# Optimization experiments

Hardware: AMD Instinct MI355X
Metric: run time of the kernel (lower is better)

## Reference

```python
import jax, jax.numpy as jnp
import numpy as np


def setup_inputs() -> dict:
    key = jax.random.key(0)
    kq, kk, kv = jax.random.split(key, 3)
    B, Lq, Lk, D = 4, 4096, 4096, 64
    return {
        "Q": jax.random.normal(kq, (B, Lq, D), dtype=jnp.float32),
        "K": jax.random.normal(kk, (B, Lk, D), dtype=jnp.float32),
        "V": jax.random.normal(kv, (B, Lk, D), dtype=jnp.float32),
    }


def reference(Q, K, V):
    # scores: [B, Lq, Lk]  (no 1/sqrt(d) scaling in the original module)
    scores = jnp.einsum("bqd,bkd->bqk", Q, K)
    attn = jax.nn.softmax(scores, axis=-1)
    # output: [B, Lq, D]
    return jnp.einsum("bqk,bkd->bqd", attn, V)
```

## Files before the change

kernel.cpp:

```cpp
#include <hip/hip_runtime.h>
#include <cmath>


#define B_    4
#define LQ    4096
#define LK    4096
#define DH    64
#define BQ    128
#define NQT2  (B_ * LQ / BQ)
#define NKVT  (LK / 128)
#define NROWS (B_ * LQ)
#define LOG2E 1.44269504088896f
#define C0    63.4785817991f

typedef _Float16 f16x8 __attribute__((ext_vector_type(8)));
typedef _Float16 f16x4 __attribute__((ext_vector_type(4)));
typedef float    f32x4 __attribute__((ext_vector_type(4)));
typedef short    s16x8 __attribute__((ext_vector_type(8)));
typedef int      i32x4 __attribute__((ext_vector_type(4)));

__device__ inline float exp2_(float x) {
#if __has_builtin(__builtin_amdgcn_exp2f)
  return __builtin_amdgcn_exp2f(x);
#else
  return exp2f(x);
#endif
}

__device__ inline unsigned pkbf16(float lo, float hi) {
  return __builtin_amdgcn_perm(__float_as_uint(hi), __float_as_uint(lo),
                               0x07060302u);
}

__device__ inline unsigned short bf16rne(float f) {
  unsigned u = __float_as_uint(f);
  return (unsigned short)((u + 0x7FFF + ((u >> 16) & 1)) >> 16);
}

__device__ inline void async16(const void* g, void* l) {
  __builtin_amdgcn_global_load_lds(
      (const __attribute__((address_space(1))) unsigned int*)g,
      (__attribute__((address_space(3))) unsigned int*)l, 16, 0, 0);
}

__global__ __launch_bounds__(256) void convert_kv4(
    const float* __restrict__ K, const float* __restrict__ V,
    _Float16* __restrict__ Kh, unsigned short* __restrict__ Vb) {
  __shared__ unsigned short Vs[64 * 68];
  const int tid = threadIdx.x;
  const int bb = blockIdx.x;
  const bool isV = bb >= 256;
  const int cc = isV ? bb - 256 : bb;
  const int b = cc >> 6, tile = (cc >> 1) & 31, half = cc & 1;
  const int kv0 = tile * 128 + half * 64;

  if (!isV) {
    for (int i = 0; i < 2; ++i) {
      int q = i * 256 + tid;
      int r = q >> 3, g = q & 7;
      const float* src = K + ((size_t)(b * LK + kv0 + r)) * DH + g * 8;
      float4 a = *(const float4*)src;
      float4 d = *(const float4*)(src + 4);
      f16x8 hv = {(_Float16)(a.x), (_Float16)(a.y), (_Float16)(a.z), (_Float16)(a.w),
                  (_Float16)(d.x), (_Float16)(d.y), (_Float16)(d.z), (_Float16)(d.w)};
      int gp = g ^ (r & 7);
      size_t dst = ((size_t)(b * 32 + tile) * 128 + half * 64 + r) * 64 + gp * 8;
      *(f16x8*)(&Kh[dst]) = hv;
    }
  } else {
    for (int i = 0; i < 4; ++i) {
      int idx = i * 256 + tid;
      int vr = idx >> 4, c4 = idx & 15;
      float4 v = *(const float4*)(&V[((size_t)(b * LK + kv0 + vr)) * DH + c4 * 4]);
      Vs[vr * 68 + c4 * 4 + 0] = bf16rne(v.x);
      Vs[vr * 68 + c4 * 4 + 1] = bf16rne(v.y);
      Vs[vr * 68 + c4 * 4 + 2] = bf16rne(v.z);
      Vs[vr * 68 + c4 * 4 + 3] = bf16rne(v.w);
    }
    __syncthreads();
    for (int i = 0; i < 2; ++i) {
      int q = i * 256 + tid;
      int d = q >> 3, gl = q & 7;
      int g = half * 8 + gl;
      unsigned short ov[8];
#pragma unroll
      for (int j = 0; j < 8; ++j) {
        int p = g * 8 + j;
        int c = p >> 5, w5 = p & 31;
        int qd = w5 >> 3, jj = w5 & 7, hh = jj >> 2, r = jj & 3;
        int sL = 32 * c + 16 * hh + 4 * qd + r - 64 * half;
        ov[j] = Vs[sL * 68 + d];
      }
      int gp = g ^ (d & 7);
      size_t dst = ((size_t)(b * 32 + tile) * 64 + d) * 128 + gp * 8;
      s16x8 o8;
#pragma unroll
      for (int j = 0; j < 8; ++j) o8[j] = (short)ov[j];
      *(s16x8*)(&Vb[dst]) = o8;
    }
  }
}

__global__ __launch_bounds__(256, 4) void ca_flash4(
    const float* __restrict__ Q, const _Float16* __restrict__ Kh,
    const unsigned short* __restrict__ Vb, float* __restrict__ Out,
    _Float16* __restrict__ Opart, float* __restrict__ Lw, int nsplit) {
  __shared__ _Float16 KsH[128 * 64];
  __shared__ unsigned short VtH[64 * 128];

  const int tid  = threadIdx.x;
  const int wave = tid >> 6;
  const int lane = tid & 63;
  const int quad = lane >> 4;
  const int l16  = lane & 15;
  const int e    = quad ^ (l16 & 7);

  const int qt    = blockIdx.x;
  const int b     = qt >> 5;
  const int qbase = (qt & 31) * BQ;
  const int sp    = blockIdx.y;
  const int t0 = (NKVT * sp) / nsplit;
  const int t1 = (NKVT * (sp + 1)) / nsplit;

  f16x8 qf[2][2];
#pragma unroll
  for (int sub = 0; sub < 2; ++sub) {
    int qrow = qbase + wave * 32 + sub * 16 + l16;
    const float* qp = Q + ((size_t)b * LQ + qrow) * DH + quad * 8;
#pragma unroll
    for (int kk = 0; kk < 2; ++kk) {
      float4 a = *(const float4*)(qp + kk * 32);
      float4 c = *(const float4*)(qp + kk * 32 + 4);
      f16x8 f = {(_Float16)(a.x * LOG2E), (_Float16)(a.y * LOG2E),
                 (_Float16)(a.z * LOG2E), (_Float16)(a.w * LOG2E),
                 (_Float16)(c.x * LOG2E), (_Float16)(c.y * LOG2E),
                 (_Float16)(c.z * LOG2E), (_Float16)(c.w * LOG2E)};
      qf[sub][kk] = f;
    }
  }

  f32x4 o[2][5];
#pragma unroll
  for (int sub = 0; sub < 2; ++sub)
#pragma unroll
    for (int td = 0; td < 5; ++td) o[sub][td] = (f32x4){0.f, 0.f, 0.f, 0.f};

  s16x8 ones;
#pragma unroll
  for (int j = 0; j < 8; ++j) ones[j] = (short)0x3F80;

  const char* kg = (const char*)Kh + ((size_t)(b * 32 + t0)) * 16384;
  const char* vg = (const char*)Vb + ((size_t)(b * 32 + t0)) * 16384;
  char* ksB = (char*)KsH;
  char* vtB = (char*)VtH;
  const char* kR = ksB + l16 * 128;
  const char* vR = vtB + l16 * 256;

  for (int tile = t0; tile < t1; ++tile) {
    __syncthreads();
    const char* sg = (wave < 2) ? (kg + wave * 8192) : (vg + (wave - 2) * 8192);
    char*       sd = (wave < 2) ? (ksB + wave * 8192) : (vtB + (wave - 2) * 8192);
#pragma unroll
    for (int i = 0; i < 8; ++i) async16(sg + i * 1024 + lane * 16, sd + i * 1024);
    __syncthreads();
    kg += 16384; vg += 16384;

#pragma unroll
    for (int c = 0; c < 4; ++c) {
      f32x4 sv[2][2];
#pragma unroll
      for (int sub = 0; sub < 2; ++sub)
#pragma unroll
        for (int tt = 0; tt < 2; ++tt)
          sv[sub][tt] = (f32x4){-C0, -C0, -C0, -C0};
#pragma unroll
      for (int kk = 0; kk < 2; ++kk) {
        int ko = (e ^ (4 * kk)) * 16;
#pragma unroll
        for (int tt = 0; tt < 2; ++tt) {
          f16x8 bk = *(const f16x8*)(kR + (2 * c + tt) * 2048 + ko);
          sv[0][tt] = __builtin_amdgcn_mfma_f32_16x16x32_f16(bk, qf[0][kk], sv[0][tt], 0, 0, 0);
          sv[1][tt] = __builtin_amdgcn_mfma_f32_16x16x32_f16(bk, qf[1][kk], sv[1][tt], 0, 0, 0);
        }
      }

      s16x8 ap[2];
#pragma unroll
      for (int sub = 0; sub < 2; ++sub) {
        unsigned u0 = pkbf16(exp2_(sv[sub][0][0]), exp2_(sv[sub][0][1]));
        unsigned u1 = pkbf16(exp2_(sv[sub][0][2]), exp2_(sv[sub][0][3]));
        unsigned u2 = pkbf16(exp2_(sv[sub][1][0]), exp2_(sv[sub][1][1]));
        unsigned u3 = pkbf16(exp2_(sv[sub][1][2]), exp2_(sv[sub][1][3]));
        i32x4 iv = {(int)u0, (int)u1, (int)u2, (int)u3};
        ap[sub] = __builtin_bit_cast(s16x8, iv);
      }

      int vo = (e ^ (4 * c)) * 16;
#pragma unroll
      for (int td = 0; td < 4; ++td) {
        s16x8 bv = *(const s16x8*)(vR + td * 4096 + vo);
        o[0][td] = __builtin_amdgcn_mfma_f32_16x16x32_bf16(ap[0], bv, o[0][td], 0, 0, 0);
        o[1][td] = __builtin_amdgcn_mfma_f32_16x16x32_bf16(ap[1], bv, o[1][td], 0, 0, 0);
      }
      o[0][4] = __builtin_amdgcn_mfma_f32_16x16x32_bf16(ap[0], ones, o[0][4], 0, 0, 0);
      o[1][4] = __builtin_amdgcn_mfma_f32_16x16x32_bf16(ap[1], ones, o[1][4], 0, 0, 0);
    }
  }

  if (nsplit == 1) {
#pragma unroll
    for (int sub = 0; sub < 2; ++sub)
#pragma unroll
      for (int r = 0; r < 4; ++r) {
        float inv = 1.0f / (o[sub][4][r] + 1e-35f);
        size_t row = (size_t)b * LQ + qbase + wave * 32 + sub * 16 + quad * 4 + r;
#pragma unroll
        for (int td = 0; td < 4; ++td)
          Out[row * DH + td * 16 + l16] = o[sub][td][r] * inv;
      }
  } else {
#pragma unroll
    for (int sub = 0; sub < 2; ++sub)
#pragma unroll
      for (int r = 0; r < 4; ++r) {
        float l = o[sub][4][r];
        float inv = 1.0f / (l + 1e-35f);
        size_t g = (size_t)qt * BQ + wave * 32 + sub * 16 + quad * 4 + r;
        size_t prow = (size_t)sp * NROWS + g;
#pragma unroll
        for (int td = 0; td < 4; ++td)
          Opart[prow * DH + td * 16 + l16] = (_Float16)(o[sub][td][r] * inv);
        if (l16 == 0) Lw[prow] = l;
      }
  }
}

__global__ __launch_bounds__(256) void ca_combine4(
    const _Float16* __restrict__ Opart, const float* __restrict__ Lw,
    float* __restrict__ Out, int nsplit) {
  const int idx = blockIdx.x * 256 + threadIdx.x;
  const int g = idx >> 4;
  const int c0 = (idx & 15) * 4;
  float den = 1e-30f;
  float a0 = 0.f, a1 = 0.f, a2 = 0.f, a3 = 0.f;
  for (int s = 0; s < nsplit; ++s) {
    size_t prow = (size_t)s * NROWS + g;
    float w = Lw[prow];
    f16x4 v = *(const f16x4*)(&Opart[prow * DH + c0]);
    a0 += w * (float)v[0]; a1 += w * (float)v[1];
    a2 += w * (float)v[2]; a3 += w * (float)v[3];
    den += w;
  }
  float inv = 1.0f / den;
  float4 ov = {a0 * inv, a1 * inv, a2 * inv, a3 * inv};
  *(float4*)(&Out[(size_t)g * DH + c0]) = ov;
}

#define LDSS 72
__global__ __launch_bounds__(256) void ca_flash_naive(
    const float* __restrict__ Q, const float* __restrict__ K,
    const float* __restrict__ V, float* __restrict__ Out) {
  __shared__ _Float16 Qs[64 * LDSS];
  __shared__ _Float16 Ks[64 * LDSS];
  __shared__ _Float16 Vt[64 * LDSS];
  __shared__ _Float16 Ps[64 * LDSS];
  const int tid = threadIdx.x, wave = tid >> 6, lane = tid & 63;
  const int quad = lane >> 4, l16 = lane & 15;
  const int b = blockIdx.x >> 6, qbase = (blockIdx.x & 63) * 64;
  for (int i = 0; i < 4; ++i) {
    int idx = (i * 256 + tid) * 4;
    int r = idx >> 6, c = idx & 63;
    float4 q4 = *(const float4*)(&Q[((size_t)b * LQ + qbase + r) * DH + c]);
    f16x4 hh = {(_Float16)q4.x, (_Float16)q4.y, (_Float16)q4.z, (_Float16)q4.w};
    *(f16x4*)(&Qs[r * LDSS + c]) = hh;
  }
  __syncthreads();
  f16x8 qf[2];
  qf[0] = *(const f16x8*)(&Qs[(wave * 16 + l16) * LDSS + quad * 8]);
  qf[1] = *(const f16x8*)(&Qs[(wave * 16 + l16) * LDSS + quad * 8 + 32]);
  float m_i[4], l_i[4];
  f32x4 o[4];
  for (int r = 0; r < 4; ++r) {
    m_i[r] = -INFINITY; l_i[r] = 0.f; o[r] = (f32x4){0.f, 0.f, 0.f, 0.f};
  }
  for (int kv0 = 0; kv0 < LK; kv0 += 64) {
    __syncthreads();
    for (int i = 0; i < 4; ++i) {
      int idx = (i * 256 + tid) * 4;
      int r = idx >> 6, c = idx & 63;
      float4 k4 = *(const float4*)(&K[((size_t)b * LK + kv0 + r) * DH + c]);
      f16x4 hh = {(_Float16)k4.x, (_Float16)k4.y, (_Float16)k4.z, (_Float16)k4.w};
      *(f16x4*)(&Ks[r * LDSS + c]) = hh;
      float4 v4 = *(const float4*)(&V[((size_t)b * LK + kv0 + r) * DH + c]);
      Vt[(c + 0) * LDSS + r] = (_Float16)v4.x;
      Vt[(c + 1) * LDSS + r] = (_Float16)v4.y;
      Vt[(c + 2) * LDSS + r] = (_Float16)v4.z;
      Vt[(c + 3) * LDSS + r] = (_Float16)v4.w;
    }
    __syncthreads();
    f32x4 sv[4];
    for (int t = 0; t < 4; ++t) sv[t] = (f32x4){0.f, 0.f, 0.f, 0.f};
    for (int kk = 0; kk < 2; ++kk)
      for (int t = 0; t < 4; ++t) {
        f16x8 bk = *(const f16x8*)(&Ks[(t * 16 + l16) * LDSS + quad * 8 + kk * 32]);
        sv[t] = __builtin_amdgcn_mfma_f32_16x16x32_f16(qf[kk], bk, sv[t], 0, 0, 0);
      }
    for (int r = 0; r < 4; ++r) {
      float mx = fmaxf(fmaxf(sv[0][r], sv[1][r]), fmaxf(sv[2][r], sv[3][r]));
      for (int off = 1; off < 16; off <<= 1) mx = fmaxf(mx, __shfl_xor(mx, off, 64));
      float mnew = fmaxf(m_i[r], mx);
      float alpha = __expf(m_i[r] - mnew);
      float rs = 0.f;
      for (int t = 0; t < 4; ++t) { float p = __expf(sv[t][r] - mnew); sv[t][r] = p; rs += p; }
      for (int off = 1; off < 16; off <<= 1) rs += __shfl_xor(rs, off, 64);
      l_i[r] = l_i[r] * alpha + rs;
      m_i[r] = mnew;
      for (int td = 0; td < 4; ++td) o[td][r] *= alpha;
    }
    for (int t = 0; t < 4; ++t)
      for (int r = 0; r < 4; ++r)
        Ps[(wave * 16 + quad * 4 + r) * LDSS + t * 16 + l16] = (_Float16)sv[t][r];
    for (int kk = 0; kk < 2; ++kk) {
      f16x8 ap = *(const f16x8*)(&Ps[(wave * 16 + l16) * LDSS + quad * 8 + kk * 32]);
      for (int td = 0; td < 4; ++td) {
        f16x8 bv = *(const f16x8*)(&Vt[(td * 16 + l16) * LDSS + quad * 8 + kk * 32]);
        o[td] = __builtin_amdgcn_mfma_f32_16x16x32_f16(ap, bv, o[td], 0, 0, 0);
      }
    }
  }
  float inv_l[4];
  for (int r = 0; r < 4; ++r) inv_l[r] = 1.0f / l_i[r];
  for (int td = 0; td < 4; ++td)
    for (int r = 0; r < 4; ++r) {
      size_t row = (size_t)b * LQ + qbase + wave * 16 + quad * 4 + r;
      Out[row * DH + td * 16 + l16] = o[td][r] * inv_l[r];
    }
}

extern "C" void kernel_launch(void* const* d_in, const int* in_sizes, int n_in,
                              void* d_out, int out_size, void* d_ws, size_t ws_size,
                              hipStream_t stream) {
  const float* Q = (const float*)d_in[0];
  const float* K = (const float*)d_in[1];
  const float* V = (const float*)d_in[2];
  float* Out = (float*)d_out;

  const size_t sKh = (size_t)B_ * LK * DH * sizeof(_Float16);
  const size_t sVb = (size_t)B_ * LK * DH * sizeof(unsigned short);
  const size_t base = sKh + sVb;
  auto opSize = [](int sp) { return (size_t)sp * NROWS * DH * sizeof(_Float16); };
  auto lwSize = [](int sp) { return (size_t)sp * NROWS * sizeof(float); };

  int split = 0;
  if (base + opSize(8) + lwSize(8) <= ws_size) split = 8;
  else if (base + opSize(6) + lwSize(6) <= ws_size) split = 6;
  else if (base + opSize(4) + lwSize(4) <= ws_size) split = 4;
  else if (base + opSize(2) + lwSize(2) <= ws_size) split = 2;
  else if (base <= ws_size) split = 1;

  char* ws = (char*)d_ws;
  if (split >= 1) {
    _Float16* Kh = (_Float16*)ws;
    unsigned short* Vb = (unsigned short*)(ws + sKh);
    convert_kv4<<<dim3(512), dim3(256), 0, stream>>>(K, V, Kh, Vb);
    if (split == 1) {
      ca_flash4<<<dim3(NQT2, 1), dim3(256), 0, stream>>>(
          Q, Kh, Vb, Out, nullptr, nullptr, 1);
    } else {
      _Float16* Op = (_Float16*)(ws + base);
      float* Lwp = (float*)(ws + base + opSize(split));
      ca_flash4<<<dim3(NQT2, split), dim3(256), 0, stream>>>(
          Q, Kh, Vb, Out, Op, Lwp, split);
      ca_combine4<<<dim3(NROWS * DH / 4 / 256), dim3(256), 0, stream>>>(
          Op, Lwp, Out, split);
    }
  } else {
    ca_flash_naive<<<dim3(256), dim3(256), 0, stream>>>(Q, K, V, Out);
  }
}
```

Before: 97.00 us.

## Fuse split-KV combine into flash kernel via last-block atomic counter

Removes the separate combine kernel launch. Each split block writes its partial output, then bumps a per-query-tile atomic counter, and the last block to arrive performs the weighted reduction into the final output. This saves one kernel launch and its dependency gap, at the cost of a memset launch, threadfences, and a serialized combine tail in the last-arriving block.

```diff
diff --git a/kernel.cpp b/kernel.cpp
--- a/kernel.cpp
+++ b/kernel.cpp
@@ -101,12 +101,14 @@
   }
 }
 
-__global__ __launch_bounds__(256, 4) void ca_flash4(
+__global__ __launch_bounds__(256, 4) void ca_flash6(
     const float* __restrict__ Q, const _Float16* __restrict__ Kh,
     const unsigned short* __restrict__ Vb, float* __restrict__ Out,
-    _Float16* __restrict__ Opart, float* __restrict__ Lw, int nsplit) {
+    _Float16* __restrict__ Opart, float* __restrict__ Lw,
+    int* __restrict__ done, int nsplit) {
   __shared__ _Float16 KsH[128 * 64];
   __shared__ unsigned short VtH[64 * 128];
+  __shared__ int sh_st;
 
   const int tid  = threadIdx.x;
   const int wave = tid >> 6;
@@ -218,42 +220,50 @@
         for (int td = 0; td < 4; ++td)
           Out[row * DH + td * 16 + l16] = o[sub][td][r] * inv;
       }
-  } else {
-#pragma unroll
-    for (int sub = 0; sub < 2; ++sub)
-#pragma unroll
-      for (int r = 0; r < 4; ++r) {
-        float l = o[sub][4][r];
-        float inv = 1.0f / (l + 1e-35f);
-        size_t g = (size_t)qt * BQ + wave * 32 + sub * 16 + quad * 4 + r;
-        size_t prow = (size_t)sp * NROWS + g;
-#pragma unroll
-        for (int td = 0; td < 4; ++td)
-          Opart[prow * DH + td * 16 + l16] = (_Float16)(o[sub][td][r] * inv);
-        if (l16 == 0) Lw[prow] = l;
-      }
-  }
-}
-
-__global__ __launch_bounds__(256) void ca_combine4(
-    const _Float16* __restrict__ Opart, const float* __restrict__ Lw,
-    float* __restrict__ Out, int nsplit) {
-  const int idx = blockIdx.x * 256 + threadIdx.x;
-  const int g = idx >> 4;
-  const int c0 = (idx & 15) * 4;
-  float den = 1e-30f;
-  float a0 = 0.f, a1 = 0.f, a2 = 0.f, a3 = 0.f;
-  for (int s = 0; s < nsplit; ++s) {
-    size_t prow = (size_t)s * NROWS + g;
-    float w = Lw[prow];
-    f16x4 v = *(const f16x4*)(&Opart[prow * DH + c0]);
-    a0 += w * (float)v[0]; a1 += w * (float)v[1];
-    a2 += w * (float)v[2]; a3 += w * (float)v[3];
-    den += w;
-  }
-  float inv = 1.0f / den;
-  float4 ov = {a0 * inv, a1 * inv, a2 * inv, a3 * inv};
-  *(float4*)(&Out[(size_t)g * DH + c0]) = ov;
+    return;
+  }
+
+#pragma unroll
+  for (int sub = 0; sub < 2; ++sub)
+#pragma unroll
+    for (int r = 0; r < 4; ++r) {
+      float l = o[sub][4][r];
+      float inv = 1.0f / (l + 1e-35f);
+      size_t g = (size_t)qt * BQ + wave * 32 + sub * 16 + quad * 4 + r;
+      size_t prow = (size_t)sp * NROWS + g;
+#pragma unroll
+      for (int td = 0; td < 4; ++td)
+        Opart[prow * DH + td * 16 + l16] = (_Float16)(o[sub][td][r] * inv);
+      if (l16 == 0) Lw[prow] = l;
+    }
+
+  __threadfence();
+  __syncthreads();
+  if (tid == 0)
+    sh_st = __hip_atomic_fetch_add(done + qt, 1, __ATOMIC_ACQ_REL,
+                                   __HIP_MEMORY_SCOPE_AGENT);
+  __syncthreads();
+  if (sh_st == nsplit - 1) {
+    __threadfence();
+    for (int i = 0; i < 8; ++i) {
+      int idx = i * 256 + tid;
+      int rr = idx >> 4;
+      int c0 = (idx & 15) * 4;
+      size_t g = (size_t)qt * BQ + rr;
+      float den = 1e-30f, a0 = 0.f, a1 = 0.f, a2 = 0.f, a3 = 0.f;
+      for (int s2 = 0; s2 < nsplit; ++s2) {
+        size_t prow = (size_t)s2 * NROWS + g;
+        float w = Lw[prow];
+        f16x4 v = *(const f16x4*)(&Opart[prow * DH + c0]);
+        a0 += w * (float)v[0]; a1 += w * (float)v[1];
+        a2 += w * (float)v[2]; a3 += w * (float)v[3];
+        den += w;
+      }
+      float inv = 1.0f / den;
+      float4 ov = {a0 * inv, a1 * inv, a2 * inv, a3 * inv};
+      *(float4*)(&Out[g * DH + c0]) = ov;
+    }
+  }
 }
 
 #define LDSS 72
@@ -350,12 +360,13 @@
   const size_t base = sKh + sVb;
   auto opSize = [](int sp) { return (size_t)sp * NROWS * DH * sizeof(_Float16); };
   auto lwSize = [](int sp) { return (size_t)sp * NROWS * sizeof(float); };
+  const size_t sDone = NQT2 * sizeof(int);
 
   int split = 0;
-  if (base + opSize(8) + lwSize(8) <= ws_size) split = 8;
-  else if (base + opSize(6) + lwSize(6) <= ws_size) split = 6;
-  else if (base + opSize(4) + lwSize(4) <= ws_size) split = 4;
-  else if (base + opSize(2) + lwSize(2) <= ws_size) split = 2;
+  if (base + opSize(8) + lwSize(8) + sDone <= ws_size) split = 8;
+  else if (base + opSize(6) + lwSize(6) + sDone <= ws_size) split = 6;
+  else if (base + opSize(4) + lwSize(4) + sDone <= ws_size) split = 4;
+  else if (base + opSize(2) + lwSize(2) + sDone <= ws_size) split = 2;
   else if (base <= ws_size) split = 1;
 
   char* ws = (char*)d_ws;
@@ -364,15 +375,15 @@
     unsigned short* Vb = (unsigned short*)(ws + sKh);
     convert_kv4<<<dim3(512), dim3(256), 0, stream>>>(K, V, Kh, Vb);
     if (split == 1) {
-      ca_flash4<<<dim3(NQT2, 1), dim3(256), 0, stream>>>(
-          Q, Kh, Vb, Out, nullptr, nullptr, 1);
+      ca_flash6<<<dim3(NQT2, 1), dim3(256), 0, stream>>>(
+          Q, Kh, Vb, Out, nullptr, nullptr, nullptr, 1);
     } else {
       _Float16* Op = (_Float16*)(ws + base);
       float* Lwp = (float*)(ws + base + opSize(split));
-      ca_flash4<<<dim3(NQT2, split), dim3(256), 0, stream>>>(
-          Q, Kh, Vb, Out, Op, Lwp, split);
-      ca_combine4<<<dim3(NROWS * DH / 4 / 256), dim3(256), 0, stream>>>(
-          Op, Lwp, Out, split);
+      int* done = (int*)(ws + base + opSize(split) + lwSize(split));
+      hipMemsetAsync(done, 0, sDone, stream);
+      ca_flash6<<<dim3(NQT2, split), dim3(256), 0, stream>>>(
+          Q, Kh, Vb, Out, Op, Lwp, done, split);
     }
   } else {
     ca_flash_naive<<<dim3(256), dim3(256), 0, stream>>>(Q, K, V, Out);
```

Result: slower. 275.9 us (+184.4%).

## Double query tile per block to 256 rows and raise KV split to 16

Applied to the files above, without the earlier changes.

Each wave now processes 64 query rows (four 16-row subtiles) instead of 32, so every K/V tile loaded into LDS feeds twice as many MFMAs, halving LDS traffic and global loads per unit of work. To keep the grid large enough with half as many query tiles, the preferred KV split count rises from 8 to 16 when workspace allows. The cost is roughly double the accumulator and score registers per thread, which may hurt occupancy under the 4-block launch bound or cause spills, plus larger partial-output writes and more combine work.

```diff
diff --git a/kernel.cpp b/kernel.cpp
--- a/kernel.cpp
+++ b/kernel.cpp
@@ -6,8 +6,8 @@
 #define LQ    4096
 #define LK    4096
 #define DH    64
-#define BQ    128
-#define NQT2  (B_ * LQ / BQ)
+#define BQ    256
+#define NQT3  (B_ * LQ / BQ)
 #define NKVT  (LK / 128)
 #define NROWS (B_ * LQ)
 #define LOG2E 1.44269504088896f
@@ -101,7 +101,7 @@
   }
 }
 
-__global__ __launch_bounds__(256, 4) void ca_flash4(
+__global__ __launch_bounds__(256, 4) void ca_flash7(
     const float* __restrict__ Q, const _Float16* __restrict__ Kh,
     const unsigned short* __restrict__ Vb, float* __restrict__ Out,
     _Float16* __restrict__ Opart, float* __restrict__ Lw, int nsplit) {
@@ -116,16 +116,16 @@
   const int e    = quad ^ (l16 & 7);
 
   const int qt    = blockIdx.x;
-  const int b     = qt >> 5;
-  const int qbase = (qt & 31) * BQ;
+  const int b     = qt >> 4;
+  const int qbase = (qt & 15) * BQ;
   const int sp    = blockIdx.y;
   const int t0 = (NKVT * sp) / nsplit;
   const int t1 = (NKVT * (sp + 1)) / nsplit;
 
-  f16x8 qf[2][2];
-#pragma unroll
-  for (int sub = 0; sub < 2; ++sub) {
-    int qrow = qbase + wave * 32 + sub * 16 + l16;
+  f16x8 qf[4][2];
+#pragma unroll
+  for (int sub = 0; sub < 4; ++sub) {
+    int qrow = qbase + wave * 64 + sub * 16 + l16;
     const float* qp = Q + ((size_t)b * LQ + qrow) * DH + quad * 8;
 #pragma unroll
     for (int kk = 0; kk < 2; ++kk) {
@@ -139,9 +139,9 @@
     }
   }
 
-  f32x4 o[2][5];
-#pragma unroll
-  for (int sub = 0; sub < 2; ++sub)
+  f32x4 o[4][5];
+#pragma unroll
+  for (int sub = 0; sub < 4; ++sub)
 #pragma unroll
     for (int td = 0; td < 5; ++td) o[sub][td] = (f32x4){0.f, 0.f, 0.f, 0.f};
 
@@ -167,9 +167,9 @@
 
 #pragma unroll
     for (int c = 0; c < 4; ++c) {
-      f32x4 sv[2][2];
-#pragma unroll
-      for (int sub = 0; sub < 2; ++sub)
+      f32x4 sv[4][2];
+#pragma unroll
+      for (int sub = 0; sub < 4; ++sub)
 #pragma unroll
         for (int tt = 0; tt < 2; ++tt)
           sv[sub][tt] = (f32x4){-C0, -C0, -C0, -C0};
@@ -179,14 +179,16 @@
 #pragma unroll
         for (int tt = 0; tt < 2; ++tt) {
           f16x8 bk = *(const f16x8*)(kR + (2 * c + tt) * 2048 + ko);
-          sv[0][tt] = __builtin_amdgcn_mfma_f32_16x16x32_f16(bk, qf[0][kk], sv[0][tt], 0, 0, 0);
-          sv[1][tt] = __builtin_amdgcn_mfma_f32_16x16x32_f16(bk, qf[1][kk], sv[1][tt], 0, 0, 0);
+#pragma unroll
+          for (int sub = 0; sub < 4; ++sub)
+            sv[sub][tt] = __builtin_amdgcn_mfma_f32_16x16x32_f16(
+                bk, qf[sub][kk], sv[sub][tt], 0, 0, 0);
         }
       }
 
-      s16x8 ap[2];
-#pragma unroll
-      for (int sub = 0; sub < 2; ++sub) {
+      s16x8 ap[4];
+#pragma unroll
+      for (int sub = 0; sub < 4; ++sub) {
         unsigned u0 = pkbf16(exp2_(sv[sub][0][0]), exp2_(sv[sub][0][1]));
         unsigned u1 = pkbf16(exp2_(sv[sub][0][2]), exp2_(sv[sub][0][3]));
         unsigned u2 = pkbf16(exp2_(sv[sub][1][0]), exp2_(sv[sub][1][1]));
@@ -199,43 +201,48 @@
 #pragma unroll
       for (int td = 0; td < 4; ++td) {
         s16x8 bv = *(const s16x8*)(vR + td * 4096 + vo);
-        o[0][td] = __builtin_amdgcn_mfma_f32_16x16x32_bf16(ap[0], bv, o[0][td], 0, 0, 0);
-        o[1][td] = __builtin_amdgcn_mfma_f32_16x16x32_bf16(ap[1], bv, o[1][td], 0, 0, 0);
-      }
-      o[0][4] = __builtin_amdgcn_mfma_f32_16x16x32_bf16(ap[0], ones, o[0][4], 0, 0, 0);
-      o[1][4] = __builtin_amdgcn_mfma_f32_16x16x32_bf16(ap[1], ones, o[1][4], 0, 0, 0);
+#pragma unroll
+        for (int sub = 0; sub < 4; ++sub)
+          o[sub][td] = __builtin_amdgcn_mfma_f32_16x16x32_bf16(
+              ap[sub], bv, o[sub][td], 0, 0, 0);
+      }
+#pragma unroll
+      for (int sub = 0; sub < 4; ++sub)
+        o[sub][4] = __builtin_amdgcn_mfma_f32_16x16x32_bf16(
+            ap[sub], ones, o[sub][4], 0, 0, 0);
     }
   }
 
   if (nsplit == 1) {
 #pragma unroll
-    for (int sub = 0; sub < 2; ++sub)
+    for (int sub = 0; sub < 4; ++sub)
 #pragma unroll
       for (int r = 0; r < 4; ++r) {
         float inv = 1.0f / (o[sub][4][r] + 1e-35f);
-        size_t row = (size_t)b * LQ + qbase + wave * 32 + sub * 16 + quad * 4 + r;
+        size_t row = (size_t)b * LQ + qbase + wave * 64 + sub * 16 + quad * 4 + r;
 #pragma unroll
         for (int td = 0; td < 4; ++td)
           Out[row * DH + td * 16 + l16] = o[sub][td][r] * inv;
       }
-  } else {
-#pragma unroll
-    for (int sub = 0; sub < 2; ++sub)
-#pragma unroll
-      for (int r = 0; r < 4; ++r) {
-        float l = o[sub][4][r];
-        float inv = 1.0f / (l + 1e-35f);
-        size_t g = (size_t)qt * BQ + wave * 32 + sub * 16 + quad * 4 + r;
-        size_t prow = (size_t)sp * NROWS + g;
-#pragma unroll
-        for (int td = 0; td < 4; ++td)
-          Opart[prow * DH + td * 16 + l16] = (_Float16)(o[sub][td][r] * inv);
-        if (l16 == 0) Lw[prow] = l;
-      }
-  }
-}
-
-__global__ __launch_bounds__(256) void ca_combine4(
+    return;
+  }
+
+#pragma unroll
+  for (int sub = 0; sub < 4; ++sub)
+#pragma unroll
+    for (int r = 0; r < 4; ++r) {
+      float l = o[sub][4][r];
+      float inv = 1.0f / (l + 1e-35f);
+      size_t g = (size_t)qt * BQ + wave * 64 + sub * 16 + quad * 4 + r;
+      size_t prow = (size_t)sp * NROWS + g;
+#pragma unroll
+      for (int td = 0; td < 4; ++td)
+        Opart[prow * DH + td * 16 + l16] = (_Float16)(o[sub][td][r] * inv);
+      if (l16 == 0) Lw[prow] = l;
+    }
+}
+
+__global__ __launch_bounds__(256) void ca_combine7(
     const _Float16* __restrict__ Opart, const float* __restrict__ Lw,
     float* __restrict__ Out, int nsplit) {
   const int idx = blockIdx.x * 256 + threadIdx.x;
@@ -352,8 +359,8 @@
   auto lwSize = [](int sp) { return (size_t)sp * NROWS * sizeof(float); };
 
   int split = 0;
-  if (base + opSize(8) + lwSize(8) <= ws_size) split = 8;
-  else if (base + opSize(6) + lwSize(6) <= ws_size) split = 6;
+  if (base + opSize(16) + lwSize(16) <= ws_size) split = 16;
+  else if (base + opSize(8) + lwSize(8) <= ws_size) split = 8;
   else if (base + opSize(4) + lwSize(4) <= ws_size) split = 4;
   else if (base + opSize(2) + lwSize(2) <= ws_size) split = 2;
   else if (base <= ws_size) split = 1;
@@ -364,14 +371,14 @@
     unsigned short* Vb = (unsigned short*)(ws + sKh);
     convert_kv4<<<dim3(512), dim3(256), 0, stream>>>(K, V, Kh, Vb);
     if (split == 1) {
-      ca_flash4<<<dim3(NQT2, 1), dim3(256), 0, stream>>>(
+      ca_flash7<<<dim3(NQT3, 1), dim3(256), 0, stream>>>(
           Q, Kh, Vb, Out, nullptr, nullptr, 1);
     } else {
       _Float16* Op = (_Float16*)(ws + base);
       float* Lwp = (float*)(ws + base + opSize(split));
-      ca_flash4<<<dim3(NQT2, split), dim3(256), 0, stream>>>(
+      ca_flash7<<<dim3(NQT3, split), dim3(256), 0, stream>>>(
           Q, Kh, Vb, Out, Op, Lwp, split);
-      ca_combine4<<<dim3(NROWS * DH / 4 / 256), dim3(256), 0, stream>>>(
+      ca_combine7<<<dim3(NROWS * DH / 4 / 256), dim3(256), 0, stream>>>(
           Op, Lwp, Out, split);
     }
   } else {
```

After: 210.8 us. 117% more time.
